# Performance work log

Measured on AMD Instinct MI355X. Metric: run time of the kernel, lower is better.

## Reference

```python
import jax, jax.numpy as jnp
import numpy as np

DIM = 1024
HID = 4096
E = 8
TOP_K = 2
LB_W = 0.01


def setup_inputs() -> dict:
    key = jax.random.key(0)
    ks = jax.random.split(key, 8)
    s = 0.02
    x = jax.random.normal(ks[0], (4, 2048, DIM), dtype=jnp.float32)
    gate_w = jax.random.normal(ks[1], (DIM, E), dtype=jnp.float32) * s
    gate_b = jnp.zeros((E,), dtype=jnp.float32)
    w1 = jax.random.normal(ks[2], (E, DIM, HID), dtype=jnp.float32) * s
    b1 = jnp.zeros((E, HID), dtype=jnp.float32)
    w2 = jax.random.normal(ks[3], (E, HID, DIM), dtype=jnp.float32) * s
    b2 = jnp.zeros((E, DIM), dtype=jnp.float32)
    return {"x": x, "gate_w": gate_w, "gate_b": gate_b,
            "w1": w1, "b1": b1, "w2": w2, "b2": b2}


def reference(x, gate_w, gate_b, w1, b1, w2, b2):
    B, S, _ = x.shape
    # gating: top-k over expert logits, softmax over the top-k logits
    gate_logits = jnp.einsum('bsd,de->bse', x, gate_w) + gate_b          # [B,S,E]
    topk_logits, topk_idx = jax.lax.top_k(gate_logits, TOP_K)            # [B,S,K]
    gating_probs = jax.nn.softmax(topk_logits, axis=-1)                  # [B,S,K]
    # scatter probs back to dense dispatch mask (top-k indices are distinct)
    dispatch = jnp.sum(jax.nn.one_hot(topk_idx, E, dtype=x.dtype)
                       * gating_probs[..., None], axis=-2)               # [B,S,E]
    # dense all-expert FFN compute, then mask + combine (faithful to source)
    h = jax.nn.gelu(jnp.einsum('bsd,edh->besh', x, w1)
                    + b1[None, :, None, :], approximate=False)           # [B,E,S,H]
    expert_out = jnp.einsum('besh,ehd->besd', h, w2) + b2[None, :, None, :]
    combined = jnp.einsum('besd,bse->bsd', expert_out, dispatch)         # [B,S,D]
    # load-balancing loss
    expert_load = jnp.sum(dispatch, axis=(0, 1)) / (B * S)               # [E]
    load_loss = LB_W * jnp.sum((expert_load - 1.0 / E) ** 2)
    return combined, load_loss, expert_load
```

## Files before the change

### kernel.cpp

```cpp
#include <hip/hip_runtime.h>
#include <math.h>
#include <stdint.h>

#define DIM   1024
#define HID   4096
#define NE    8
#define NTOK  8192
#define MAXROWS 17408
#define LB_W  0.01f

typedef unsigned short u16;
typedef unsigned int   u32;

typedef __bf16 bf16x8 __attribute__((ext_vector_type(8)));
typedef float  f32x4  __attribute__((ext_vector_type(4)));
typedef u16    u16x8  __attribute__((ext_vector_type(8)));

__device__ __forceinline__ u16 f2b(float f) {
    union { float f; u32 i; } v; v.f = f;
    u32 u = v.i;
    return (u16)((u + 0x7FFFu + ((u >> 16) & 1u)) >> 16);
}

__global__ __launch_bounds__(256)
void gate_kernel(const float* __restrict__ x, const float* __restrict__ gw,
                 const float* __restrict__ gb, u32* __restrict__ tokE,
                 float2* __restrict__ tokP, int* __restrict__ cnt,
                 float* __restrict__ eload)
{
    __shared__ float se[NE];
    __shared__ int   sc[NE];
    const int tid = threadIdx.x;
    if (tid < NE) { se[tid] = 0.f; sc[tid] = 0; }
    __syncthreads();
    const int lane = tid & 63, wid = tid >> 6;
    for (int j = 0; j < 8; ++j) {
        const int t = blockIdx.x * 32 + wid * 8 + j;
        float s[NE];
#pragma unroll
        for (int ee = 0; ee < NE; ++ee) s[ee] = 0.f;
        const float* xt = x + (size_t)t * DIM + lane * 16;
#pragma unroll
        for (int q = 0; q < 4; ++q) {
            const float4 xv = *(const float4*)(xt + q * 4);
            const float xf[4] = {xv.x, xv.y, xv.z, xv.w};
#pragma unroll
            for (int u = 0; u < 4; ++u) {
                const int d = lane * 16 + q * 4 + u;
                const float4 g0 = *(const float4*)(gw + d * 8);
                const float4 g1 = *(const float4*)(gw + d * 8 + 4);
                s[0] += xf[u] * g0.x; s[1] += xf[u] * g0.y;
                s[2] += xf[u] * g0.z; s[3] += xf[u] * g0.w;
                s[4] += xf[u] * g1.x; s[5] += xf[u] * g1.y;
                s[6] += xf[u] * g1.z; s[7] += xf[u] * g1.w;
            }
        }
#pragma unroll
        for (int ee = 0; ee < NE; ++ee) {
#pragma unroll
            for (int off = 32; off >= 1; off >>= 1)
                s[ee] += __shfl_xor(s[ee], off);
        }
        if (lane == 0) {
            float l[NE];
#pragma unroll
            for (int ee = 0; ee < NE; ++ee) l[ee] = s[ee] + gb[ee];
            int e0 = 0;
#pragma unroll
            for (int ee = 1; ee < NE; ++ee) if (l[ee] > l[e0]) e0 = ee;
            int e1 = (e0 == 0) ? 1 : 0;
#pragma unroll
            for (int ee = 0; ee < NE; ++ee)
                if (ee != e0 && l[ee] > l[e1]) e1 = ee;
            const float p0 = 1.f / (1.f + expf(l[e1] - l[e0]));
            const float p1 = 1.f - p0;
            tokE[t] = (u32)e0 | ((u32)e1 << 16);
            tokP[t] = make_float2(p0, p1);
            atomicAdd(&se[e0], p0);
            atomicAdd(&se[e1], p1);
            atomicAdd(&sc[e0], 1);
            atomicAdd(&sc[e1], 1);
        }
    }
    __syncthreads();
    if (tid < NE) {
        atomicAdd(&eload[tid], se[tid]);
        atomicAdd(&cnt[tid], sc[tid]);
    }
}

__global__ void offsets_kernel(const int* __restrict__ cnt, int* __restrict__ offs,
                               int* __restrict__ rowtok, float* __restrict__ rowp)
{
    int c[NE], off[NE], cap[NE];
    int o = 0;
#pragma unroll
    for (int e = 0; e < NE; ++e) {
        c[e] = cnt[e];
        cap[e] = (c[e] + 127) & ~127;
        off[e] = o;
        o += cap[e];
    }
    if (threadIdx.x < NE) offs[threadIdx.x] = off[threadIdx.x];
    for (int e = 0; e < NE; ++e)
        for (int i = c[e] + (int)threadIdx.x; i < cap[e]; i += 64) {
            rowtok[off[e] + i] = 0;
            rowp[off[e] + i]   = 0.f;
        }
}

__global__ __launch_bounds__(256)
void scatter_kernel(const u32* __restrict__ tokE, const float2* __restrict__ tokP,
                    const int* __restrict__ offs, int* __restrict__ cnt2,
                    int* __restrict__ rowtok, float* __restrict__ rowp)
{
    __shared__ int lc[NE];
    __shared__ int lb[NE];
    const int tid = threadIdx.x;
    if (tid < NE) lc[tid] = 0;
    __syncthreads();
    const int t = blockIdx.x * 256 + tid;
    const u32 ep = tokE[t];
    const float2 p = tokP[t];
    const int e0 = (int)(ep & 0xFFFFu), e1 = (int)(ep >> 16);
    const int q0 = atomicAdd(&lc[e0], 1);
    const int q1 = atomicAdd(&lc[e1], 1);
    __syncthreads();
    if (tid < NE) lb[tid] = atomicAdd(&cnt2[tid], lc[tid]);
    __syncthreads();
    const int r0 = offs[e0] + lb[e0] + q0;
    rowtok[r0] = t; rowp[r0] = p.x;
    const int r1 = offs[e1] + lb[e1] + q1;
    rowtok[r1] = t; rowp[r1] = p.y;
}

__global__ __launch_bounds__(256)
void transpose_kernel(const float* __restrict__ in, u16* __restrict__ out,
                      int R, int C)
{
    __shared__ float tile[32][33];
    const int e = blockIdx.z;
    const float* pin = in + (size_t)e * R * C;
    u16* pout = out + (size_t)e * R * C;
    const int c0 = blockIdx.x * 32, r0 = blockIdx.y * 32;
#pragma unroll
    for (int i = 0; i < 4; ++i) {
        const int r = threadIdx.y + i * 8;
        tile[r][threadIdx.x] = pin[(size_t)(r0 + r) * C + c0 + threadIdx.x];
    }
    __syncthreads();
#pragma unroll
    for (int i = 0; i < 4; ++i) {
        const int r = threadIdx.y + i * 8;
        pout[(size_t)(c0 + r) * R + r0 + threadIdx.x] = f2b(tile[threadIdx.x][r]);
    }
}

__global__ __launch_bounds__(256, 2)
void gemm1_kernel(const float* __restrict__ x, const u16* __restrict__ w1t,
                  const float* __restrict__ b1, const int* __restrict__ cnt,
                  const int* __restrict__ offs, const int* __restrict__ rowtok,
                  u16* __restrict__ h)
{
    const int e = blockIdx.z;
    const int ne = cnt[e];
    const int mt = blockIdx.y;
    if (mt * 128 >= ne) return;
    const int nt = blockIdx.x;
    const int rowbase = offs[e] + mt * 128;

    __shared__ u16 lA[128 * 64];
    __shared__ u16 lB[128 * 64];

    const int tid = threadIdx.x;
    const int lane = tid & 63;

    const u16* wB = w1t + (size_t)e * HID * DIM + (size_t)nt * 128 * DIM;

    const float* agp[4];
    const u16*   bgp[4];
#pragma unroll
    for (int c = 0; c < 4; ++c) {
        const int lin = tid + c * 256;
        const int row = lin >> 3, k8 = lin & 7;
        const int tok = rowtok[rowbase + row];
        agp[c] = x + (size_t)tok * DIM + k8 * 8;
        bgp[c] = wB + (size_t)row * DIM + k8 * 8;
    }

    f32x4 acc[4][4];
#pragma unroll
    for (int i = 0; i < 4; ++i)
#pragma unroll
        for (int j = 0; j < 4; ++j)
            acc[i][j] = (f32x4){0.f, 0.f, 0.f, 0.f};

    const int wid = tid >> 6;
    const int wm = (wid >> 1) * 64;
    const int wn = (wid & 1) * 64;

    for (int k0 = 0; k0 < DIM; k0 += 64) {
        float4 fa[4][2];
        u16x8  rb[4];
#pragma unroll
        for (int c = 0; c < 4; ++c) {
            fa[c][0] = *(const float4*)(agp[c] + k0);
            fa[c][1] = *(const float4*)(agp[c] + k0 + 4);
            rb[c]    = *(const u16x8*)(bgp[c] + k0);
        }
        __syncthreads();
#pragma unroll
        for (int c = 0; c < 4; ++c) {
            u16x8 ra;
            ra[0] = f2b(fa[c][0].x); ra[1] = f2b(fa[c][0].y);
            ra[2] = f2b(fa[c][0].z); ra[3] = f2b(fa[c][0].w);
            ra[4] = f2b(fa[c][1].x); ra[5] = f2b(fa[c][1].y);
            ra[6] = f2b(fa[c][1].z); ra[7] = f2b(fa[c][1].w);
            *(u16x8*)&lA[(tid + c * 256) * 8] = ra;
            *(u16x8*)&lB[(tid + c * 256) * 8] = rb[c];
        }
        __syncthreads();
#pragma unroll
        for (int ks = 0; ks < 2; ++ks) {
            const int kin = ks * 32 + (lane >> 4) * 8;
            bf16x8 av[4], bv[4];
#pragma unroll
            for (int f = 0; f < 4; ++f) {
                av[f] = *(const bf16x8*)&lA[(wm + f * 16 + (lane & 15)) * 64 + kin];
                bv[f] = *(const bf16x8*)&lB[(wn + f * 16 + (lane & 15)) * 64 + kin];
            }
#pragma unroll
            for (int i = 0; i < 4; ++i)
#pragma unroll
                for (int j = 0; j < 4; ++j)
                    acc[i][j] = __builtin_amdgcn_mfma_f32_16x16x32_bf16(
                        av[i], bv[j], acc[i][j], 0, 0, 0);
        }
    }

    const int col = lane & 15;
    const int rq = (lane >> 4) * 4;
    const float* b1e = b1 + e * HID;
#pragma unroll
    for (int j = 0; j < 4; ++j) {
        const int hcol = nt * 128 + wn + j * 16 + col;
        const float bias = b1e[hcol];
#pragma unroll
        for (int i = 0; i < 4; ++i) {
            const int mrow = wm + i * 16 + rq;
#pragma unroll
            for (int r = 0; r < 4; ++r) {
                float v = acc[i][j][r] + bias;
                v = 0.5f * v * (1.f + erff(v * 0.70710678118f));
                h[(size_t)(rowbase + mrow + r) * HID + hcol] = f2b(v);
            }
        }
    }
}

__global__ __launch_bounds__(256, 2)
void gemm2_kernel(const u16* __restrict__ h, const u16* __restrict__ w2t,
                  const float* __restrict__ b2, const int* __restrict__ cnt,
                  const int* __restrict__ offs, const int* __restrict__ rowtok,
                  const float* __restrict__ rowp, float* __restrict__ outc)
{
    const int e = blockIdx.z;
    const int ne = cnt[e];
    const int mt = blockIdx.y;
    if (mt * 128 >= ne) return;
    const int nt = blockIdx.x;
    const int rowbase = offs[e] + mt * 128;

    __shared__ u16 lA[128 * 64];
    __shared__ u16 lB[128 * 64];

    const int tid = threadIdx.x;
    const int lane = tid & 63;

    const u16* wB = w2t + (size_t)e * DIM * HID + (size_t)nt * 128 * HID;

    const u16* agp[4];
    const u16* bgp[4];
#pragma unroll
    for (int c = 0; c < 4; ++c) {
        const int lin = tid + c * 256;
        const int row = lin >> 3, k8 = lin & 7;
        agp[c] = h  + (size_t)(rowbase + row) * HID + k8 * 8;
        bgp[c] = wB + (size_t)row * HID + k8 * 8;
    }

    f32x4 acc[4][4];
#pragma unroll
    for (int i = 0; i < 4; ++i)
#pragma unroll
        for (int j = 0; j < 4; ++j)
            acc[i][j] = (f32x4){0.f, 0.f, 0.f, 0.f};

    const int wid = tid >> 6;
    const int wm = (wid >> 1) * 64;
    const int wn = (wid & 1) * 64;

    for (int k0 = 0; k0 < HID; k0 += 64) {
        u16x8 ra[4], rb[4];
#pragma unroll
        for (int c = 0; c < 4; ++c) {
            ra[c] = *(const u16x8*)(agp[c] + k0);
            rb[c] = *(const u16x8*)(bgp[c] + k0);
        }
        __syncthreads();
#pragma unroll
        for (int c = 0; c < 4; ++c) {
            *(u16x8*)&lA[(tid + c * 256) * 8] = ra[c];
            *(u16x8*)&lB[(tid + c * 256) * 8] = rb[c];
        }
        __syncthreads();
#pragma unroll
        for (int ks = 0; ks < 2; ++ks) {
            const int kin = ks * 32 + (lane >> 4) * 8;
            bf16x8 av[4], bv[4];
#pragma unroll
            for (int f = 0; f < 4; ++f) {
                av[f] = *(const bf16x8*)&lA[(wm + f * 16 + (lane & 15)) * 64 + kin];
                bv[f] = *(const bf16x8*)&lB[(wn + f * 16 + (lane & 15)) * 64 + kin];
            }
#pragma unroll
            for (int i = 0; i < 4; ++i)
#pragma unroll
                for (int j = 0; j < 4; ++j)
                    acc[i][j] = __builtin_amdgcn_mfma_f32_16x16x32_bf16(
                        av[i], bv[j], acc[i][j], 0, 0, 0);
        }
    }

    const int col = lane & 15;
    const int rq = (lane >> 4) * 4;
    const float* b2e = b2 + e * DIM;
    float biasv[4];
#pragma unroll
    for (int j = 0; j < 4; ++j)
        biasv[j] = b2e[nt * 128 + wn + j * 16 + col];
#pragma unroll
    for (int i = 0; i < 4; ++i) {
#pragma unroll
        for (int r = 0; r < 4; ++r) {
            const int rg = rowbase + wm + i * 16 + rq + r;
            const float p = rowp[rg];
            const int tok = rowtok[rg];
            float* dst = outc + (size_t)tok * DIM + nt * 128 + wn + col;
#pragma unroll
            for (int j = 0; j < 4; ++j)
                atomicAdd(dst + j * 16, (acc[i][j][r] + biasv[j]) * p);
        }
    }
}

__global__ void tail_kernel(const float* __restrict__ eload, float* __restrict__ out)
{
    if (threadIdx.x == 0) {
        float loss = 0.f;
        float le[NE];
#pragma unroll
        for (int e = 0; e < NE; ++e) {
            le[e] = eload[e] * (1.f / (float)NTOK);
            const float d = le[e] - 1.f / (float)NE;
            loss += d * d;
        }
        loss *= LB_W;
        out[(size_t)NTOK * DIM] = loss;
#pragma unroll
        for (int e = 0; e < NE; ++e)
            out[(size_t)NTOK * DIM + 1 + e] = le[e];
    }
}

extern "C" void kernel_launch(void* const* d_in, const int* in_sizes, int n_in,
                              void* d_out, int out_size, void* d_ws, size_t ws_size,
                              hipStream_t stream)
{
    const float* x  = (const float*)d_in[0];
    const float* gw = (const float*)d_in[1];
    const float* gb = (const float*)d_in[2];
    const float* w1 = (const float*)d_in[3];
    const float* b1 = (const float*)d_in[4];
    const float* w2 = (const float*)d_in[5];
    const float* b2 = (const float*)d_in[6];
    float* out = (float*)d_out;
    char* ws = (char*)d_ws;

    int*    cnt    = (int*)   (ws + 0);
    int*    cnt2   = (int*)   (ws + 32);
    int*    offs   = (int*)   (ws + 64);
    float*  eload  = (float*) (ws + 96);
    u32*    tokE   = (u32*)   (ws + 128);
    float2* tokP   = (float2*)(ws + 32896);
    int*    rowtok = (int*)   (ws + 98432);
    float*  rowp   = (float*) (ws + 168064);
    u16*    w1t    = (u16*)   (ws + 237824);
    u16*    w2t    = (u16*)   (ws + 67346688);
    u16*    h      = (u16*)   (ws + 134455552);

    hipMemsetAsync(ws, 0, 128, stream);
    hipMemsetAsync(out, 0, (size_t)NTOK * DIM * sizeof(float), stream);

    transpose_kernel<<<dim3(HID / 32, DIM / 32, NE), dim3(32, 8), 0, stream>>>(
        w1, w1t, DIM, HID);
    transpose_kernel<<<dim3(DIM / 32, HID / 32, NE), dim3(32, 8), 0, stream>>>(
        w2, w2t, HID, DIM);
    gate_kernel<<<NTOK / 32, 256, 0, stream>>>(x, gw, gb, tokE, tokP, cnt, eload);
    offsets_kernel<<<1, 64, 0, stream>>>(cnt, offs, rowtok, rowp);
    scatter_kernel<<<NTOK / 256, 256, 0, stream>>>(tokE, tokP, offs, cnt2, rowtok, rowp);
    gemm1_kernel<<<dim3(HID / 128, 64, NE), 256, 0, stream>>>(
        x, w1t, b1, cnt, offs, rowtok, h);
    gemm2_kernel<<<dim3(DIM / 128, 64, NE), 256, 0, stream>>>(
        h, w2t, b2, cnt, offs, rowtok, rowp, out);
    tail_kernel<<<1, 64, 0, stream>>>(eload, out);
}
```

Before: 933.0 us.

## Pre-convert x to bf16, use direct global-to-LDS loads with XOR swizzle

The gate kernel now also writes a bf16 copy of x, so gemm1 no longer loads fp32 activations and converts them inside the k-loop. Both grouped GEMMs switch from register-staged tile loads to global_load_lds direct-to-LDS transfers, with an XOR swizzle on the k-chunk to avoid LDS bank conflicts. The grid is reordered so M tiles vary fastest, and the occupancy hint rises from 2 to 4 blocks per CU. The aim is to cut VGPR staging, conversion work and bank conflicts, at the cost of an extra bf16 buffer for x and no overlap between loads and compute.

Result: slower. 1.309 ms (+40.3%).

```diff
diff --git a/kernel.cpp b/kernel.cpp
--- a/kernel.cpp
+++ b/kernel.cpp
@@ -16,6 +16,9 @@
 typedef float  f32x4  __attribute__((ext_vector_type(4)));
 typedef u16    u16x8  __attribute__((ext_vector_type(8)));
 
+typedef const __attribute__((address_space(1))) void* gas_t;
+typedef __attribute__((address_space(3))) void* las_t;
+
 __device__ __forceinline__ u16 f2b(float f) {
     union { float f; u32 i; } v; v.f = f;
     u32 u = v.i;
@@ -26,7 +29,7 @@
 void gate_kernel(const float* __restrict__ x, const float* __restrict__ gw,
                  const float* __restrict__ gb, u32* __restrict__ tokE,
                  float2* __restrict__ tokP, int* __restrict__ cnt,
-                 float* __restrict__ eload)
+                 float* __restrict__ eload, u16* __restrict__ xb)
 {
     __shared__ float se[NE];
     __shared__ int   sc[NE];
@@ -40,10 +43,13 @@
 #pragma unroll
         for (int ee = 0; ee < NE; ++ee) s[ee] = 0.f;
         const float* xt = x + (size_t)t * DIM + lane * 16;
+        u16 xc[16];
 #pragma unroll
         for (int q = 0; q < 4; ++q) {
             const float4 xv = *(const float4*)(xt + q * 4);
             const float xf[4] = {xv.x, xv.y, xv.z, xv.w};
+            xc[q * 4 + 0] = f2b(xv.x); xc[q * 4 + 1] = f2b(xv.y);
+            xc[q * 4 + 2] = f2b(xv.z); xc[q * 4 + 3] = f2b(xv.w);
 #pragma unroll
             for (int u = 0; u < 4; ++u) {
                 const int d = lane * 16 + q * 4 + u;
@@ -55,6 +61,9 @@
                 s[6] += xf[u] * g1.z; s[7] += xf[u] * g1.w;
             }
         }
+        u16* xbo = xb + (size_t)t * DIM + lane * 16;
+        *(u16x8*)(xbo)     = *(const u16x8*)&xc[0];
+        *(u16x8*)(xbo + 8) = *(const u16x8*)&xc[8];
 #pragma unroll
         for (int ee = 0; ee < NE; ++ee) {
 #pragma unroll
@@ -156,17 +165,17 @@
     }
 }
 
-__global__ __launch_bounds__(256, 2)
-void gemm1_kernel(const float* __restrict__ x, const u16* __restrict__ w1t,
+__global__ __launch_bounds__(256, 4)
+void gemm1_kernel(const u16* __restrict__ xb, const u16* __restrict__ w1t,
                   const float* __restrict__ b1, const int* __restrict__ cnt,
                   const int* __restrict__ offs, const int* __restrict__ rowtok,
                   u16* __restrict__ h)
 {
     const int e = blockIdx.z;
     const int ne = cnt[e];
-    const int mt = blockIdx.y;
+    const int mt = blockIdx.x;
     if (mt * 128 >= ne) return;
-    const int nt = blockIdx.x;
+    const int nt = blockIdx.y;
     const int rowbase = offs[e] + mt * 128;
 
     __shared__ u16 lA[128 * 64];
@@ -174,17 +183,19 @@
 
     const int tid = threadIdx.x;
     const int lane = tid & 63;
+    const int wid = tid >> 6;
 
     const u16* wB = w1t + (size_t)e * HID * DIM + (size_t)nt * 128 * DIM;
 
-    const float* agp[4];
-    const u16*   bgp[4];
+    const u16* agp[4];
+    const u16* bgp[4];
 #pragma unroll
     for (int c = 0; c < 4; ++c) {
         const int lin = tid + c * 256;
-        const int row = lin >> 3, k8 = lin & 7;
+        const int row = lin >> 3;
+        const int k8 = (lin & 7) ^ (row & 7);
         const int tok = rowtok[rowbase + row];
-        agp[c] = x + (size_t)tok * DIM + k8 * 8;
+        agp[c] = xb + (size_t)tok * DIM + k8 * 8;
         bgp[c] = wB + (size_t)row * DIM + k8 * 8;
     }
 
@@ -195,39 +206,31 @@
         for (int j = 0; j < 4; ++j)
             acc[i][j] = (f32x4){0.f, 0.f, 0.f, 0.f};
 
-    const int wid = tid >> 6;
     const int wm = (wid >> 1) * 64;
     const int wn = (wid & 1) * 64;
+    const int rsub = lane & 15;
+    const int sw = lane & 7;
+    const int cq = lane >> 4;
 
     for (int k0 = 0; k0 < DIM; k0 += 64) {
-        float4 fa[4][2];
-        u16x8  rb[4];
+        __syncthreads();
 #pragma unroll
         for (int c = 0; c < 4; ++c) {
-            fa[c][0] = *(const float4*)(agp[c] + k0);
-            fa[c][1] = *(const float4*)(agp[c] + k0 + 4);
-            rb[c]    = *(const u16x8*)(bgp[c] + k0);
+            __builtin_amdgcn_global_load_lds((gas_t)(agp[c] + k0),
+                (las_t)&lA[(tid + c * 256) * 8], 16, 0, 0);
+            __builtin_amdgcn_global_load_lds((gas_t)(bgp[c] + k0),
+                (las_t)&lB[(tid + c * 256) * 8], 16, 0, 0);
         }
         __syncthreads();
 #pragma unroll
-        for (int c = 0; c < 4; ++c) {
-            u16x8 ra;
-            ra[0] = f2b(fa[c][0].x); ra[1] = f2b(fa[c][0].y);
-            ra[2] = f2b(fa[c][0].z); ra[3] = f2b(fa[c][0].w);
-            ra[4] = f2b(fa[c][1].x); ra[5] = f2b(fa[c][1].y);
-            ra[6] = f2b(fa[c][1].z); ra[7] = f2b(fa[c][1].w);
-            *(u16x8*)&lA[(tid + c * 256) * 8] = ra;
-            *(u16x8*)&lB[(tid + c * 256) * 8] = rb[c];
-        }
-        __syncthreads();
-#pragma unroll
         for (int ks = 0; ks < 2; ++ks) {
-            const int kin = ks * 32 + (lane >> 4) * 8;
+            const int cc = ks * 4 + cq;
+            const int js = (cc ^ sw) * 8;
             bf16x8 av[4], bv[4];
 #pragma unroll
             for (int f = 0; f < 4; ++f) {
-                av[f] = *(const bf16x8*)&lA[(wm + f * 16 + (lane & 15)) * 64 + kin];
-                bv[f] = *(const bf16x8*)&lB[(wn + f * 16 + (lane & 15)) * 64 + kin];
+                av[f] = *(const bf16x8*)&lA[(wm + f * 16 + rsub) * 64 + js];
+                bv[f] = *(const bf16x8*)&lB[(wn + f * 16 + rsub) * 64 + js];
             }
 #pragma unroll
             for (int i = 0; i < 4; ++i)
@@ -258,7 +261,7 @@
     }
 }
 
-__global__ __launch_bounds__(256, 2)
+__global__ __launch_bounds__(256, 4)
 void gemm2_kernel(const u16* __restrict__ h, const u16* __restrict__ w2t,
                   const float* __restrict__ b2, const int* __restrict__ cnt,
                   const int* __restrict__ offs, const int* __restrict__ rowtok,
@@ -266,9 +269,9 @@
 {
     const int e = blockIdx.z;
     const int ne = cnt[e];
-    const int mt = blockIdx.y;
+    const int mt = blockIdx.x;
     if (mt * 128 >= ne) return;
-    const int nt = blockIdx.x;
+    const int nt = blockIdx.y;
     const int rowbase = offs[e] + mt * 128;
 
     __shared__ u16 lA[128 * 64];
@@ -276,6 +279,7 @@
 
     const int tid = threadIdx.x;
     const int lane = tid & 63;
+    const int wid = tid >> 6;
 
     const u16* wB = w2t + (size_t)e * DIM * HID + (size_t)nt * 128 * HID;
 
@@ -284,7 +288,8 @@
 #pragma unroll
     for (int c = 0; c < 4; ++c) {
         const int lin = tid + c * 256;
-        const int row = lin >> 3, k8 = lin & 7;
+        const int row = lin >> 3;
+        const int k8 = (lin & 7) ^ (row & 7);
         agp[c] = h  + (size_t)(rowbase + row) * HID + k8 * 8;
         bgp[c] = wB + (size_t)row * HID + k8 * 8;
     }
@@ -296,32 +301,31 @@
         for (int j = 0; j < 4; ++j)
             acc[i][j] = (f32x4){0.f, 0.f, 0.f, 0.f};
 
-    const int wid = tid >> 6;
     const int wm = (wid >> 1) * 64;
     const int wn = (wid & 1) * 64;
+    const int rsub = lane & 15;
+    const int sw = lane & 7;
+    const int cq = lane >> 4;
 
     for (int k0 = 0; k0 < HID; k0 += 64) {
-        u16x8 ra[4], rb[4];
+        __syncthreads();
 #pragma unroll
         for (int c = 0; c < 4; ++c) {
-            ra[c] = *(const u16x8*)(agp[c] + k0);
-            rb[c] = *(const u16x8*)(bgp[c] + k0);
+            __builtin_amdgcn_global_load_lds((gas_t)(agp[c] + k0),
+                (las_t)&lA[(tid + c * 256) * 8], 16, 0, 0);
+            __builtin_amdgcn_global_load_lds((gas_t)(bgp[c] + k0),
+                (las_t)&lB[(tid + c * 256) * 8], 16, 0, 0);
         }
         __syncthreads();
 #pragma unroll
-        for (int c = 0; c < 4; ++c) {
-            *(u16x8*)&lA[(tid + c * 256) * 8] = ra[c];
-            *(u16x8*)&lB[(tid + c * 256) * 8] = rb[c];
-        }
-        __syncthreads();
-#pragma unroll
         for (int ks = 0; ks < 2; ++ks) {
-            const int kin = ks * 32 + (lane >> 4) * 8;
+            const int cc = ks * 4 + cq;
+            const int js = (cc ^ sw) * 8;
             bf16x8 av[4], bv[4];
 #pragma unroll
             for (int f = 0; f < 4; ++f) {
-                av[f] = *(const bf16x8*)&lA[(wm + f * 16 + (lane & 15)) * 64 + kin];
-                bv[f] = *(const bf16x8*)&lB[(wn + f * 16 + (lane & 15)) * 64 + kin];
+                av[f] = *(const bf16x8*)&lA[(wm + f * 16 + rsub) * 64 + js];
+                bv[f] = *(const bf16x8*)&lB[(wn + f * 16 + rsub) * 64 + js];
             }
 #pragma unroll
             for (int i = 0; i < 4; ++i)
@@ -395,9 +399,10 @@
     float2* tokP   = (float2*)(ws + 32896);
     int*    rowtok = (int*)   (ws + 98432);
     float*  rowp   = (float*) (ws + 168064);
-    u16*    w1t    = (u16*)   (ws + 237824);
-    u16*    w2t    = (u16*)   (ws + 67346688);
-    u16*    h      = (u16*)   (ws + 134455552);
+    u16*    xb     = (u16*)   (ws + 237824);
+    u16*    w1t    = (u16*)   (ws + 17015040);
+    u16*    w2t    = (u16*)   (ws + 84123904);
+    u16*    h      = (u16*)   (ws + 151232768);
 
     hipMemsetAsync(ws, 0, 128, stream);
     hipMemsetAsync(out, 0, (size_t)NTOK * DIM * sizeof(float), stream);
@@ -406,12 +411,12 @@
         w1, w1t, DIM, HID);
     transpose_kernel<<<dim3(DIM / 32, HID / 32, NE), dim3(32, 8), 0, stream>>>(
         w2, w2t, HID, DIM);
-    gate_kernel<<<NTOK / 32, 256, 0, stream>>>(x, gw, gb, tokE, tokP, cnt, eload);
+    gate_kernel<<<NTOK / 32, 256, 0, stream>>>(x, gw, gb, tokE, tokP, cnt, eload, xb);
     offsets_kernel<<<1, 64, 0, stream>>>(cnt, offs, rowtok, rowp);
     scatter_kernel<<<NTOK / 256, 256, 0, stream>>>(tokE, tokP, offs, cnt2, rowtok, rowp);
-    gemm1_kernel<<<dim3(HID / 128, 64, NE), 256, 0, stream>>>(
-        x, w1t, b1, cnt, offs, rowtok, h);
-    gemm2_kernel<<<dim3(DIM / 128, 64, NE), 256, 0, stream>>>(
+    gemm1_kernel<<<dim3(64, HID / 128, NE), 256, 0, stream>>>(
+        xb, w1t, b1, cnt, offs, rowtok, h);
+    gemm2_kernel<<<dim3(64, DIM / 128, NE), 256, 0, stream>>>(
         h, w2t, b2, cnt, offs, rowtok, rowp, out);
     tail_kernel<<<1, 64, 0, stream>>>(eload, out);
 }
```
